# Performance work log

Measured on AMD Instinct MI355X. Metric: run time of the kernel, lower is better.

## Reference

```python
import jax, jax.numpy as jnp
import numpy as np

EMBED_DIM = 768
EMBED_PER_TYPE = EMBED_DIM // 6  # 128


def setup_inputs() -> dict:
    key = jax.random.key(0)
    ks = jax.random.split(key, 6)
    d = EMBED_PER_TYPE
    return {
        "price_w": jax.random.normal(ks[0], (1, d), dtype=jnp.float32),
        "size_w": jax.random.normal(ks[1], (1, d), dtype=jnp.float32),
        "exchange_w": jax.random.normal(ks[2], (4, d), dtype=jnp.float32),
        "pair_w": jax.random.normal(ks[3], (8, d), dtype=jnp.float32),
        "level_w": jax.random.normal(ks[4], (16, d), dtype=jnp.float32),
        "time_w": jax.random.normal(ks[5], (32, d), dtype=jnp.float32),
        "num_features": 131072,
    }


def reference(price_w, size_w, exchange_w, pair_w, level_w, time_w, num_features):
    # Vectorized version of the per-feature loop: indices are 0, 0, i%3, i%7, i%15, i%31.
    idx = jnp.arange(num_features)
    parts = [
        jnp.broadcast_to(price_w[0], (num_features, EMBED_PER_TYPE)),
        jnp.broadcast_to(size_w[0], (num_features, EMBED_PER_TYPE)),
        exchange_w[idx % 3],
        pair_w[idx % 7],
        level_w[idx % 15],
        time_w[idx % 31],
    ]
    return jnp.concatenate(parts, axis=-1)  # [num_features, embed_dim]
```

## Files before the change

### kernel.cpp

```cpp
#include <hip/hip_runtime.h>

#define EMBED_PER_TYPE 128
#define EMBED_DIM 768
#define ROWS_PER_BLOCK 4

__global__ __launch_bounds__(256) void smart_embedding_kernel(
    const float* __restrict__ price_w,
    const float* __restrict__ size_w,
    const float* __restrict__ exchange_w,
    const float* __restrict__ pair_w,
    const float* __restrict__ level_w,
    const float* __restrict__ time_w,
    const int* __restrict__ nf_ptr,
    float* __restrict__ out)
{
    const int nf = *nf_ptr;
    const int tid  = threadIdx.x;
    const int wave = tid >> 6;
    const int lane = tid & 63;
    const unsigned row = blockIdx.x * ROWS_PER_BLOCK + wave;
    if (row >= (unsigned)nf) return;

    const float* bases[6];
    bases[0] = price_w;
    bases[1] = size_w;
    bases[2] = exchange_w + (row % 3u)  * EMBED_PER_TYPE;
    bases[3] = pair_w     + (row % 7u)  * EMBED_PER_TYPE;
    bases[4] = level_w    + (row % 15u) * EMBED_PER_TYPE;
    bases[5] = time_w     + (row % 31u) * EMBED_PER_TYPE;

    float* __restrict__ orow = out + (size_t)row * EMBED_DIM;
    const int off = (lane & 31) * 4;
    const bool hi = (lane >= 32);

#pragma unroll
    for (int k = 0; k < 3; ++k) {
        const float* base = hi ? bases[2 * k + 1] : bases[2 * k];
        float4 v = *reinterpret_cast<const float4*>(base + off);
        *reinterpret_cast<float4*>(orow + (k * 64 + lane) * 4) = v;
    }
}

extern "C" void kernel_launch(void* const* d_in, const int* in_sizes, int n_in,
                              void* d_out, int out_size, void* d_ws, size_t ws_size,
                              hipStream_t stream) {
    const float* price_w    = (const float*)d_in[0];
    const float* size_w     = (const float*)d_in[1];
    const float* exchange_w = (const float*)d_in[2];
    const float* pair_w     = (const float*)d_in[3];
    const float* level_w    = (const float*)d_in[4];
    const float* time_w     = (const float*)d_in[5];
    const int*   nf_ptr     = (const int*)d_in[6];
    float* out = (float*)d_out;

    const int rows = out_size / EMBED_DIM;
    const int blocks = (rows + ROWS_PER_BLOCK - 1) / ROWS_PER_BLOCK;

    smart_embedding_kernel<<<blocks, 256, 0, stream>>>(
        price_w, size_w, exchange_w, pair_w, level_w, time_w, nf_ptr, out);
}
```

Measured before the change: 421.4 us.

## Process multiple rows per wave with nontemporal stores and incremental modulo indices

Each wave now writes a chunk of 16 consecutive rows instead of one. The constant price/size vector is loaded once per wave, and the modulo indices are advanced incrementally rather than recomputed with divisions. All stores use nontemporal hints so the large streaming output does not pollute the cache. The grid shrinks by a factor of 16, which cuts launch and scheduling overhead but leaves fewer waves to hide store latency. The row count now comes from the output size instead of reading num_features on the device.

```diff
diff --git a/kernel.cpp b/kernel.cpp
--- a/kernel.cpp
+++ b/kernel.cpp
@@ -1,61 +1,69 @@
 #include <hip/hip_runtime.h>
 
-#define EMBED_PER_TYPE 128
-#define EMBED_DIM 768
-#define ROWS_PER_BLOCK 4
+#define ROW_F4 192
+#define CHUNK  16
+
+typedef float v4f __attribute__((ext_vector_type(4)));
 
 __global__ __launch_bounds__(256) void smart_embedding_kernel(
-    const float* __restrict__ price_w,
-    const float* __restrict__ size_w,
-    const float* __restrict__ exchange_w,
-    const float* __restrict__ pair_w,
-    const float* __restrict__ level_w,
-    const float* __restrict__ time_w,
-    const int* __restrict__ nf_ptr,
-    float* __restrict__ out)
+    const v4f* __restrict__ price_w,
+    const v4f* __restrict__ size_w,
+    const v4f* __restrict__ exchange_w,
+    const v4f* __restrict__ pair_w,
+    const v4f* __restrict__ level_w,
+    const v4f* __restrict__ time_w,
+    v4f* __restrict__ out,
+    int rows)
 {
-    const int nf = *nf_ptr;
     const int tid  = threadIdx.x;
     const int wave = tid >> 6;
     const int lane = tid & 63;
-    const unsigned row = blockIdx.x * ROWS_PER_BLOCK + wave;
-    if (row >= (unsigned)nf) return;
+    const int off  = lane & 31;
+    const bool hi  = lane >= 32;
 
-    const float* bases[6];
-    bases[0] = price_w;
-    bases[1] = size_w;
-    bases[2] = exchange_w + (row % 3u)  * EMBED_PER_TYPE;
-    bases[3] = pair_w     + (row % 7u)  * EMBED_PER_TYPE;
-    bases[4] = level_w    + (row % 15u) * EMBED_PER_TYPE;
-    bases[5] = time_w     + (row % 31u) * EMBED_PER_TYPE;
+    int r0 = (blockIdx.x * 4 + wave) * CHUNK;
+    if (r0 >= rows) return;
+    const int rend = (r0 + CHUNK < rows) ? r0 + CHUNK : rows;
 
-    float* __restrict__ orow = out + (size_t)row * EMBED_DIM;
-    const int off = (lane & 31) * 4;
-    const bool hi = (lane >= 32);
+    const v4f v0 = hi ? size_w[off] : price_w[off];
 
-#pragma unroll
-    for (int k = 0; k < 3; ++k) {
-        const float* base = hi ? bases[2 * k + 1] : bases[2 * k];
-        float4 v = *reinterpret_cast<const float4*>(base + off);
-        *reinterpret_cast<float4*>(orow + (k * 64 + lane) * 4) = v;
+    const v4f* base1 = hi ? pair_w : exchange_w;
+    const v4f* base2 = hi ? time_w : level_w;
+    const int p1 = hi ? 7  : 3;
+    const int p2 = hi ? 31 : 15;
+
+    int m1 = r0 % p1;
+    int m2 = r0 % p2;
+
+    v4f* orow = out + (size_t)r0 * ROW_F4 + lane;
+
+#pragma unroll 4
+    for (int r = r0; r < rend; ++r) {
+        v4f v1 = base1[m1 * 32 + off];
+        v4f v2 = base2[m2 * 32 + off];
+        __builtin_nontemporal_store(v0, orow);
+        __builtin_nontemporal_store(v1, orow + 64);
+        __builtin_nontemporal_store(v2, orow + 128);
+        orow += ROW_F4;
+        m1 = (m1 + 1 == p1) ? 0 : m1 + 1;
+        m2 = (m2 + 1 == p2) ? 0 : m2 + 1;
     }
 }
 
 extern "C" void kernel_launch(void* const* d_in, const int* in_sizes, int n_in,
                               void* d_out, int out_size, void* d_ws, size_t ws_size,
                               hipStream_t stream) {
-    const float* price_w    = (const float*)d_in[0];
-    const float* size_w     = (const float*)d_in[1];
-    const float* exchange_w = (const float*)d_in[2];
-    const float* pair_w     = (const float*)d_in[3];
-    const float* level_w    = (const float*)d_in[4];
-    const float* time_w     = (const float*)d_in[5];
-    const int*   nf_ptr     = (const int*)d_in[6];
-    float* out = (float*)d_out;
+    const v4f* price_w    = (const v4f*)d_in[0];
+    const v4f* size_w     = (const v4f*)d_in[1];
+    const v4f* exchange_w = (const v4f*)d_in[2];
+    const v4f* pair_w     = (const v4f*)d_in[3];
+    const v4f* level_w    = (const v4f*)d_in[4];
+    const v4f* time_w     = (const v4f*)d_in[5];
+    v4f* out = (v4f*)d_out;
 
-    const int rows = out_size / EMBED_DIM;
-    const int blocks = (rows + ROWS_PER_BLOCK - 1) / ROWS_PER_BLOCK;
+    const int rows = out_size / 768;
+    const int blocks = (rows + 4 * CHUNK - 1) / (4 * CHUNK);
 
     smart_embedding_kernel<<<blocks, 256, 0, stream>>>(
-        price_w, size_w, exchange_w, pair_w, level_w, time_w, nf_ptr, out);
+        price_w, size_w, exchange_w, pair_w, level_w, time_w, out, rows);
 }
```

Measured after the change: 406.2 us. 1.04x faster.
